# Kernel optimization log

Measured on AMD Instinct MI355X. Metric: run time of the kernel, lower is better.

## Reference

```python
import jax, jax.numpy as jnp
import numpy as np

B, N, DIN, DOUT = 8, 2048, 64, 64
TAU = 2.0            # softmax temperature
NEG_SLOPE = 0.2      # LeakyReLU slope
EDGE_P = 0.02        # adjacency density


def setup_inputs() -> dict:
    key = jax.random.key(0)
    kx, ka, kw, ks, kd = jax.random.split(key, 5)
    x = jax.random.normal(kx, (B, N, DIN), dtype=jnp.float32)
    # sparse 0/1 road-graph adjacency with self-loops, stored dense as in the module
    A = (jax.random.uniform(ka, (B, N, N)) < EDGE_P).astype(jnp.float32)
    A = jnp.maximum(A, jnp.eye(N, dtype=jnp.float32)[None])
    # learned parameters (nn.Linear without bias): W [DIN,DOUT], a_src/a_dst [DOUT]
    W = jax.random.normal(kw, (DIN, DOUT), dtype=jnp.float32) / np.sqrt(DIN)
    a_src = jax.random.normal(ks, (DOUT,), dtype=jnp.float32) / np.sqrt(DOUT)
    a_dst = jax.random.normal(kd, (DOUT,), dtype=jnp.float32) / np.sqrt(DOUT)
    return {"x": x, "A": A, "W": W, "a_src": a_src, "a_dst": a_dst}


def reference(x, A, W, a_src, a_dst):
    Wx = jnp.einsum("bni,io->bno", x, W)          # [B,N,DOUT]
    e_src = jnp.einsum("bno,o->bn", Wx, a_src)     # [B,N]
    e_dst = jnp.einsum("bno,o->bn", Wx, a_dst)     # [B,N]
    e = e_src[:, :, None] + e_dst[:, None, :]      # [B,N,N]
    e = jnp.where(e > 0, e, NEG_SLOPE * e)         # LeakyReLU(0.2)
    e = jnp.where(A < 1e-9, -jnp.inf, e)           # mask non-edges
    alpha = jax.nn.softmax(e / TAU, axis=-1)
    alpha = jnp.nan_to_num(alpha, nan=0.0)         # rows with no neighbours -> 0
    return jnp.einsum("bnm,bmo->bno", alpha, Wx)   # [B,N,DOUT]
```

## Files before the change

kernel.cpp:

```cpp
#include <hip/hip_runtime.h>
#include <hip/hip_bf16.h>


#define BQ 8
#define NQ 2048
#define DQ 64
#define TAUQ 2.0f
#define SLOPEQ 0.2f
#define CAP 136

typedef float f4v __attribute__((ext_vector_type(4)));

__global__ __launch_bounds__(256) void gat_p1_scan(
    const float* __restrict__ x, const float* __restrict__ A,
    const float* __restrict__ W,
    const float* __restrict__ a_src, const float* __restrict__ a_dst,
    float* __restrict__ Wx, float* __restrict__ esrc, float* __restrict__ edst,
    unsigned* __restrict__ emask)
{
    const int t = threadIdx.x;
    const int wave = t >> 6, lane = t & 63;
    const int idx = blockIdx.x >> 1;
    const int row = idx * 4 + wave;

    if (blockIdx.x & 1) {
        const float* __restrict__ Arow = A + (size_t)row * NQ;
        unsigned lm = 0;
#pragma unroll
        for (int k = 0; k < 8; ++k) {
            f4v a4 = __builtin_nontemporal_load(
                reinterpret_cast<const f4v*>(Arow + k * 256 + 4 * lane));
#pragma unroll
            for (int j = 0; j < 4; ++j)
                if (a4[j] >= 1e-9f) lm |= 1u << (k * 4 + j);
        }
        emask[row * 64 + lane] = lm;
        return;
    }

    __shared__ float Wl[64 * 64];
    __shared__ float xl[4][64];
    for (int i = t; i < 64 * 64; i += 256) Wl[i] = W[i];
    xl[wave][lane] = x[row * DQ + lane];
    __syncthreads();

    float acc = 0.f;
#pragma unroll
    for (int i = 0; i < 64; ++i)
        acc += xl[wave][i] * Wl[i * 64 + lane];
    Wx[row * DQ + lane] = acc;

    float ps = acc * a_src[lane];
    float pd = acc * a_dst[lane];
#pragma unroll
    for (int o = 32; o > 0; o >>= 1) {
        ps += __shfl_xor(ps, o);
        pd += __shfl_xor(pd, o);
    }
    if (lane == 0) { esrc[row] = ps; edst[row] = pd; }
}

__global__ __launch_bounds__(256) void gat_apply(
    const unsigned* __restrict__ emask, const float* __restrict__ Wx,
    const float* __restrict__ esrc, const float* __restrict__ edst,
    float* __restrict__ out)
{
    const int t = threadIdx.x;
    const int wave = t >> 6, lane = t & 63;
    const int row = blockIdx.x * 4 + wave;
    const int b = row >> 11;
    const float* __restrict__ ed = edst + b * NQ;
    const float  es = esrc[row];

    __shared__ int2 eL[4][CAP];

    unsigned lm = emask[row * 64 + lane];

    const int cnt = __popc(lm);
    int incl = cnt;
#pragma unroll
    for (int o = 1; o < 64; o <<= 1) {
        int v = __shfl_up(incl, o);
        if (lane >= o) incl += v;
    }
    int total = __shfl(incl, 63);
    if (total > CAP - 8) total = CAP - 8;
    int base = incl - cnt;
    unsigned mrem = lm;
    while (mrem) {
        const int pos = __builtin_ctz(mrem);
        mrem &= mrem - 1;
        if (base < CAP - 8)
            eL[wave][base].x = ((pos >> 2) << 8) + 4 * lane + (pos & 3);
        ++base;
    }

    float mx = -INFINITY;
    for (int i = lane; i < total; i += 64) {
        const int m = eL[wave][i].x;
        float e = es + ed[m];
        e = e > 0.f ? e : SLOPEQ * e;
        eL[wave][i].y = __float_as_int(e);
        mx = fmaxf(mx, e);
    }
#pragma unroll
    for (int o = 32; o > 0; o >>= 1) mx = fmaxf(mx, __shfl_xor(mx, o));

    const float invtau = 1.0f / TAUQ;
    float s = 0.f;
    for (int i = lane; i < total; i += 64) {
        const float e = __int_as_float(eL[wave][i].y);
        const float p = __expf((e - mx) * invtau);
        eL[wave][i].y = __float_as_int(p);
        s += p;
    }
#pragma unroll
    for (int o = 32; o > 0; o >>= 1) s += __shfl_xor(s, o);
    const float inv = (s > 0.f) ? 1.0f / s : 0.f;

    const int pad = (8 - (total & 7)) & 7;
    if (lane < pad) eL[wave][total + lane] = make_int2(0, 0);
    const int padded = total + pad;

    const float* __restrict__ Wxb = Wx + (size_t)b * NQ * DQ;
    float acc = 0.f;
    for (int i = 0; i < padded; i += 8) {
        const int2 e0 = eL[wave][i + 0], e1 = eL[wave][i + 1];
        const int2 e2 = eL[wave][i + 2], e3 = eL[wave][i + 3];
        const int2 e4 = eL[wave][i + 4], e5 = eL[wave][i + 5];
        const int2 e6 = eL[wave][i + 6], e7 = eL[wave][i + 7];
        const float w0 = Wxb[((size_t)(unsigned)e0.x << 6) + lane];
        const float w1 = Wxb[((size_t)(unsigned)e1.x << 6) + lane];
        const float w2 = Wxb[((size_t)(unsigned)e2.x << 6) + lane];
        const float w3 = Wxb[((size_t)(unsigned)e3.x << 6) + lane];
        const float w4 = Wxb[((size_t)(unsigned)e4.x << 6) + lane];
        const float w5 = Wxb[((size_t)(unsigned)e5.x << 6) + lane];
        const float w6 = Wxb[((size_t)(unsigned)e6.x << 6) + lane];
        const float w7 = Wxb[((size_t)(unsigned)e7.x << 6) + lane];
        acc += __int_as_float(e0.y) * w0;
        acc += __int_as_float(e1.y) * w1;
        acc += __int_as_float(e2.y) * w2;
        acc += __int_as_float(e3.y) * w3;
        acc += __int_as_float(e4.y) * w4;
        acc += __int_as_float(e5.y) * w5;
        acc += __int_as_float(e6.y) * w6;
        acc += __int_as_float(e7.y) * w7;
    }
    out[(size_t)row * DQ + lane] = acc * inv;
}

extern "C" void kernel_launch(void* const* d_in, const int* in_sizes, int n_in,
                              void* d_out, int out_size, void* d_ws, size_t ws_size,
                              hipStream_t stream) {
    const float* x     = (const float*)d_in[0];
    const float* A     = (const float*)d_in[1];
    const float* W     = (const float*)d_in[2];
    const float* a_src = (const float*)d_in[3];
    const float* a_dst = (const float*)d_in[4];
    float* out = (float*)d_out;

    float*    Wx    = (float*)d_ws;
    float*    esrc  = Wx + (size_t)BQ * NQ * DQ;
    float*    edst  = esrc + (size_t)BQ * NQ;
    unsigned* emask = (unsigned*)(edst + (size_t)BQ * NQ);

    gat_p1_scan<<<BQ * NQ / 2, 256, 0, stream>>>(x, A, W, a_src, a_dst,
                                                 Wx, esrc, edst, emask);
    gat_apply<<<BQ * NQ / 4, 256, 0, stream>>>(emask, Wx, esrc, edst, out);
}
```

Measured before the change: 49.87 us.

## Scan 8 adjacency rows per wave with double-buffered loads and rebalance block split

The first kernel now gives each scan wave 8 consecutive adjacency rows and double-buffers the loads, prefetching the next row while building the bitmask for the current one. The grid is reorganised so one in nine blocks scans and eight compute Wx, replacing the earlier alternating one-to-one split. This cuts the scan block count and per-block overhead and raises memory-level parallelism, but each scanning wave now does much more serial work and nontemporal loads become plain loads. The mask test also changes from >= 1e-9 to != 0, which differs from the reference for very small or negative adjacency values.

```diff
diff --git a/kernel.cpp b/kernel.cpp
--- a/kernel.cpp
+++ b/kernel.cpp
@@ -8,8 +8,28 @@
 #define TAUQ 2.0f
 #define SLOPEQ 0.2f
 #define CAP 136
+#define SRPW 8
 
 typedef float f4v __attribute__((ext_vector_type(4)));
+
+__device__ __forceinline__ void issue_row(const float* __restrict__ Arow,
+                                          int lane, f4v a[8])
+{
+#pragma unroll
+    for (int k = 0; k < 8; ++k)
+        a[k] = *reinterpret_cast<const f4v*>(Arow + k * 256 + 4 * lane);
+}
+
+__device__ __forceinline__ unsigned mask_of(const f4v a[8])
+{
+    unsigned lm = 0;
+#pragma unroll
+    for (int k = 0; k < 8; ++k)
+#pragma unroll
+        for (int j = 0; j < 4; ++j)
+            if (a[k][j] != 0.f) lm |= 1u << (k * 4 + j);
+    return lm;
+}
 
 __global__ __launch_bounds__(256) void gat_p1_scan(
     const float* __restrict__ x, const float* __restrict__ A,
@@ -20,23 +40,26 @@
 {
     const int t = threadIdx.x;
     const int wave = t >> 6, lane = t & 63;
-    const int idx = blockIdx.x >> 1;
-    const int row = idx * 4 + wave;
+    const int g = blockIdx.x;
 
-    if (blockIdx.x & 1) {
-        const float* __restrict__ Arow = A + (size_t)row * NQ;
-        unsigned lm = 0;
+    if (g % 9 == 0) {
+        const int w = (g / 9) * 4 + wave;
+        const int row0 = w * SRPW;
+        const float* __restrict__ Ab = A + (size_t)row0 * NQ;
+        f4v aA[8], aB[8];
+        issue_row(Ab, lane, aA);
 #pragma unroll
-        for (int k = 0; k < 8; ++k) {
-            f4v a4 = __builtin_nontemporal_load(
-                reinterpret_cast<const f4v*>(Arow + k * 256 + 4 * lane));
-#pragma unroll
-            for (int j = 0; j < 4; ++j)
-                if (a4[j] >= 1e-9f) lm |= 1u << (k * 4 + j);
+        for (int i = 0; i < SRPW; ++i) {
+            if (i + 1 < SRPW)
+                issue_row(Ab + (size_t)(i + 1) * NQ, lane, (i & 1) ? aA : aB);
+            const unsigned lm = mask_of((i & 1) ? aB : aA);
+            emask[(size_t)(row0 + i) * 64 + lane] = lm;
         }
-        emask[row * 64 + lane] = lm;
         return;
     }
+
+    const int pidx = (g / 9) * 8 + (g % 9) - 1;
+    const int row = pidx * 4 + wave;
 
     __shared__ float Wl[64 * 64];
     __shared__ float xl[4][64];
@@ -74,7 +97,7 @@
 
     __shared__ int2 eL[4][CAP];
 
-    unsigned lm = emask[row * 64 + lane];
+    unsigned lm = emask[(size_t)row * 64 + lane];
 
     const int cnt = __popc(lm);
     int incl = cnt;
@@ -164,7 +187,7 @@
     float*    edst  = esrc + (size_t)BQ * NQ;
     unsigned* emask = (unsigned*)(edst + (size_t)BQ * NQ);
 
-    gat_p1_scan<<<BQ * NQ / 2, 256, 0, stream>>>(x, A, W, a_src, a_dst,
-                                                 Wx, esrc, edst, emask);
+    gat_p1_scan<<<4608, 256, 0, stream>>>(x, A, W, a_src, a_dst,
+                                          Wx, esrc, edst, emask);
     gat_apply<<<BQ * NQ / 4, 256, 0, stream>>>(emask, Wx, esrc, edst, out);
 }
```

After: 43.68 us. 12.4% less time.
